# Kernel optimization log

Measured on AMD Instinct MI355X. Metric: run time of the kernel, lower is better.

Reference implementation:

```python
import jax, jax.numpy as jnp
import numpy as np

D_MODEL = 1024
H = 16
D_K = D_MODEL // H
B, S = 2, 2048
NEG = -1e9


def setup_inputs() -> dict:
    key = jax.random.key(0)
    ks = jax.random.split(key, 8)
    scale = 1.0 / np.sqrt(D_MODEL)
    q = jax.random.normal(ks[0], (B, S, D_MODEL), dtype=jnp.float32)
    k = jax.random.normal(ks[1], (B, S, D_MODEL), dtype=jnp.float32)
    v = jax.random.normal(ks[2], (B, S, D_MODEL), dtype=jnp.float32)
    # causal 0/1 mask, broadcastable to [B, h, S, S]
    mask = jnp.tril(jnp.ones((S, S), dtype=jnp.int32))[None, None, :, :]
    w_q = jax.random.normal(ks[3], (D_MODEL, D_MODEL), dtype=jnp.float32) * scale
    w_k = jax.random.normal(ks[4], (D_MODEL, D_MODEL), dtype=jnp.float32) * scale
    w_v = jax.random.normal(ks[5], (D_MODEL, D_MODEL), dtype=jnp.float32) * scale
    w_o = jax.random.normal(ks[6], (D_MODEL, D_MODEL), dtype=jnp.float32) * scale
    return {"q": q, "k": k, "v": v, "mask": mask,
            "w_q": w_q, "w_k": w_k, "w_v": w_v, "w_o": w_o}


def reference(q, k, v, mask, w_q, w_k, w_v, w_o):
    # projections (no bias)
    def split_heads(x):
        Bn, Sn, _ = x.shape
        return x.reshape(Bn, Sn, H, D_K).transpose(0, 2, 1, 3)  # [B,h,S,d_k]

    qh = split_heads(q @ w_q)
    kh = split_heads(k @ w_k)
    vh = split_heads(v @ w_v)

    scores = jnp.einsum('bhqd,bhkd->bhqk', qh, kh) / jnp.sqrt(
        jnp.asarray(D_K, dtype=qh.dtype))
    scores = jnp.where(mask == 0, jnp.asarray(NEG, dtype=scores.dtype), scores)
    attn = jax.nn.softmax(scores, axis=-1)  # dropout rate 0.0 -> identity
    x = jnp.einsum('bhqk,bhkd->bhqd', attn, vh)  # [B,h,S,d_k]
    x = x.transpose(0, 2, 1, 3).reshape(q.shape[0], q.shape[1], D_MODEL)
    return x @ w_o
```

## Files before the change

kernel.cpp:

```cpp
#include <hip/hip_runtime.h>

#define D_MODEL 1024
#define NH 16
#define DK 64
#define BB 2
#define SS 2048
#define M_TOT (BB*SS)

typedef float f32x4 __attribute__((ext_vector_type(4)));
typedef float f32x16 __attribute__((ext_vector_type(16)));
typedef __bf16 bf16x8 __attribute__((ext_vector_type(8)));
typedef unsigned int u32;

#define QSCALE 0.1803368801f
#define DEFER_THR 11.5416f

__device__ __forceinline__ unsigned short f2bf(float f){
  unsigned int u = __float_as_uint(f);
  unsigned int r = (u + 0x7fffu + ((u >> 16) & 1u)) >> 16;
  return (unsigned short)r;
}

__device__ __forceinline__ void gload_lds16(const void* g, void* l){
  __builtin_amdgcn_global_load_lds((const __attribute__((address_space(1))) void*)g,
                                   (__attribute__((address_space(3))) void*)l,
                                   16, 0, 0);
}

__device__ __forceinline__ void swap_half(u32 a, u32 b, int hi, u32& x, u32& y){
#if __has_builtin(__builtin_amdgcn_permlane32_swap)
  typedef unsigned int uint2v __attribute__((ext_vector_type(2)));
  uint2v r = __builtin_amdgcn_permlane32_swap(a, b, false, false);
  x = r.x; y = r.y;
#else
  u32 as = __shfl_xor(a, 32);
  u32 bs = __shfl_xor(b, 32);
  x = hi ? bs : a;
  y = hi ? b  : as;
#endif
}

__global__ __launch_bounds__(256) void cvt3_bf16(const float* __restrict__ q,
                                                 const float* __restrict__ k,
                                                 const float* __restrict__ v,
                                                 unsigned short* __restrict__ qb,
                                                 unsigned short* __restrict__ kb,
                                                 unsigned short* __restrict__ vb){
  const int which = blockIdx.y;
  const float* in = (which == 0) ? q : (which == 1) ? k : v;
  unsigned short* out = (which == 0) ? qb : (which == 1) ? kb : vb;
  int i = blockIdx.x * 256 + threadIdx.x;
  float4 f = ((const float4*)in)[i];
  ushort4 o;
  o.x = f2bf(f.x); o.y = f2bf(f.y); o.z = f2bf(f.z); o.w = f2bf(f.w);
  ((ushort4*)out)[i] = o;
}

__global__ __launch_bounds__(256) void transpose_cvt4(const float* __restrict__ wq,
                                                      const float* __restrict__ wk,
                                                      const float* __restrict__ wv,
                                                      const float* __restrict__ wo,
                                                      unsigned short* __restrict__ WqkvT,
                                                      unsigned short* __restrict__ woT){
  __shared__ float tile[64][65];
  const int which = blockIdx.z;
  const float* w = (which == 0) ? wq : (which == 1) ? wk : (which == 2) ? wv : wo;
  unsigned short* wt = (which == 3) ? woT : (WqkvT + (size_t)which * 1024 * 1024);
  const int N = D_MODEL;
  const int bx = blockIdx.x * 64;
  const int by = blockIdx.y * 64;
  const int t = threadIdx.x;
  #pragma unroll
  for (int i = 0; i < 16; ++i){
    int idx = t + i * 256;
    int r = idx >> 6, c = idx & 63;
    tile[r][c] = w[(size_t)(by + r) * N + bx + c];
  }
  __syncthreads();
  #pragma unroll
  for (int i = 0; i < 16; ++i){
    int idx = t + i * 256;
    int r = idx >> 6, c = idx & 63;
    wt[(size_t)(bx + r) * N + by + c] = f2bf(tile[c][r]);
  }
}

__global__ __launch_bounds__(256) void gemm_qkv(const unsigned short* __restrict__ Aq,
                                                const unsigned short* __restrict__ Ak,
                                                const unsigned short* __restrict__ Av,
                                                const unsigned short* __restrict__ WT,
                                                unsigned short* __restrict__ Qh,
                                                unsigned short* __restrict__ Kh,
                                                unsigned short* __restrict__ VhT){
  __shared__ unsigned short Al[2][128 * 32];
  __shared__ unsigned short Bl[2][128 * 32];
  const int tid = threadIdx.x;
  const int wid = tid >> 6, lane = tid & 63;
  const int lr = lane & 15, lg = lane >> 4;
  const int wm = wid >> 1, wn = wid & 1;
  const int bm = blockIdx.x, bn = blockIdx.y;
  const int seg = bn >> 3;
  const unsigned short* A = (seg == 0) ? Aq : (seg == 1) ? Ak : Av;
  const int K = D_MODEL;

  f32x4 acc[4][4];
  #pragma unroll
  for (int i = 0; i < 4; ++i)
    #pragma unroll
    for (int j = 0; j < 4; ++j)
      acc[i][j] = (f32x4){0.f, 0.f, 0.f, 0.f};

  auto stage = [&](int buf, int kt){
    #pragma unroll
    for (int r = 0; r < 2; ++r){
      int vt = tid + r * 256;
      int row = vt >> 2, c8 = (vt & 3) * 8;
      gload_lds16(A  + (size_t)(bm * 128 + row) * K + kt * 32 + c8,
                  &Al[buf][(wid << 9) + r * 2048]);
      gload_lds16(WT + (size_t)(bn * 128 + row) * K + kt * 32 + c8,
                  &Bl[buf][(wid << 9) + r * 2048]);
    }
  };

  stage(0, 0);
  int cur = 0;
  for (int kt = 0; kt < 32; ++kt){
    __syncthreads();
    if (kt + 1 < 32) stage(cur ^ 1, kt + 1);
    bf16x8 af[4], bfr[4];
    #pragma unroll
    for (int i = 0; i < 4; ++i)
      af[i] = *(const bf16x8*)&Al[cur][(wm * 64 + i * 16 + lr) * 32 + lg * 8];
    #pragma unroll
    for (int j = 0; j < 4; ++j)
      bfr[j] = *(const bf16x8*)&Bl[cur][(wn * 64 + j * 16 + lr) * 32 + lg * 8];
    #pragma unroll
    for (int i = 0; i < 4; ++i)
      #pragma unroll
      for (int j = 0; j < 4; ++j)
        acc[i][j] = __builtin_amdgcn_mfma_f32_16x16x32_bf16(af[i], bfr[j], acc[i][j], 0, 0, 0);
    cur ^= 1;
  }

  if (seg < 2){
    unsigned short* O = (seg == 0) ? Qh : Kh;
    const float sc = (seg == 0) ? QSCALE : 1.0f;
    #pragma unroll
    for (int i = 0; i < 4; ++i){
      int row0 = bm * 128 + wm * 64 + i * 16 + lg * 4;
      #pragma unroll
      for (int j = 0; j < 4; ++j){
        int colseg = (bn & 7) * 128 + wn * 64 + j * 16 + lr;
        int h = colseg >> 6, dk = colseg & 63;
        #pragma unroll
        for (int p = 0; p < 4; ++p){
          int rowm = row0 + p;
          int b = rowm >> 11, s = rowm & 2047;
          O[((size_t)(b * NH + h) * SS + s) * DK + dk] = f2bf(acc[i][j][p] * sc);
        }
      }
    }
  } else {
    #pragma unroll
    for (int i = 0; i < 4; ++i){
      int row0 = bm * 128 + wm * 64 + i * 16 + lg * 4;
      int b = row0 >> 11, s = row0 & 2047;
      #pragma unroll
      for (int j = 0; j < 4; ++j){
        int colseg = (bn & 7) * 128 + wn * 64 + j * 16 + lr;
        int h = colseg >> 6, dk = colseg & 63;
        ushort4 o4;
        o4.x = f2bf(acc[i][j][0]); o4.y = f2bf(acc[i][j][1]);
        o4.z = f2bf(acc[i][j][2]); o4.w = f2bf(acc[i][j][3]);
        *(ushort4*)&VhT[((size_t)(b * NH + h) * DK + dk) * SS + s] = o4;
      }
    }
  }
}

__global__ __launch_bounds__(256) void gemm_o64(const unsigned short* __restrict__ A,
                                                const unsigned short* __restrict__ Bt,
                                                float* __restrict__ O){
  __shared__ unsigned short Al[2][64 * 32];
  __shared__ unsigned short Bl[2][128 * 32];
  const int tid = threadIdx.x;
  const int wid = tid >> 6, lane = tid & 63;
  const int lr = lane & 15, lg = lane >> 4;
  const int wm = wid >> 1, wn = wid & 1;
  const int bm = blockIdx.x, bn = blockIdx.y;
  const int K = D_MODEL;

  f32x4 acc[2][4];
  #pragma unroll
  for (int i = 0; i < 2; ++i)
    #pragma unroll
    for (int j = 0; j < 4; ++j)
      acc[i][j] = (f32x4){0.f, 0.f, 0.f, 0.f};

  auto stage = [&](int buf, int kt){
    {
      int row = tid >> 2, c8 = (tid & 3) * 8;
      gload_lds16(A + (size_t)(bm * 64 + row) * K + kt * 32 + c8,
                  &Al[buf][wid << 9]);
    }
    #pragma unroll
    for (int r = 0; r < 2; ++r){
      int vt = tid + r * 256;
      int row = vt >> 2, c8 = (vt & 3) * 8;
      gload_lds16(Bt + (size_t)(bn * 128 + row) * K + kt * 32 + c8,
                  &Bl[buf][(wid << 9) + r * 2048]);
    }
  };

  stage(0, 0);
  int cur = 0;
  for (int kt = 0; kt < 32; ++kt){
    __syncthreads();
    if (kt + 1 < 32) stage(cur ^ 1, kt + 1);
    bf16x8 af[2], bfr[4];
    #pragma unroll
    for (int i = 0; i < 2; ++i)
      af[i] = *(const bf16x8*)&Al[cur][(wm * 32 + i * 16 + lr) * 32 + lg * 8];
    #pragma unroll
    for (int j = 0; j < 4; ++j)
      bfr[j] = *(const bf16x8*)&Bl[cur][(wn * 64 + j * 16 + lr) * 32 + lg * 8];
    #pragma unroll
    for (int i = 0; i < 2; ++i)
      #pragma unroll
      for (int j = 0; j < 4; ++j)
        acc[i][j] = __builtin_amdgcn_mfma_f32_16x16x32_bf16(af[i], bfr[j], acc[i][j], 0, 0, 0);
    cur ^= 1;
  }

  #pragma unroll
  for (int i = 0; i < 2; ++i){
    int row0 = bm * 64 + wm * 32 + i * 16 + lg * 4;
    #pragma unroll
    for (int j = 0; j < 4; ++j){
      int col = bn * 128 + wn * 64 + j * 16 + lr;
      #pragma unroll
      for (int p = 0; p < 4; ++p)
        O[(size_t)(row0 + p) * D_MODEL + col] = acc[i][j][p];
    }
  }
}

__global__ __launch_bounds__(256) void attn_kernel(const unsigned short* __restrict__ Qh,
                                                   const unsigned short* __restrict__ Kh,
                                                   const unsigned short* __restrict__ VhT,
                                                   unsigned short* __restrict__ Oc){
  __shared__ unsigned short SL[4][4096];
  const int bh = blockIdx.x;
  const int qblk = 31 - blockIdx.y;
  const int tid = threadIdx.x, wid = tid >> 6, lane = tid & 63;
  const int ln = lane & 31, hi = lane >> 5;
  const int qh = wid & 1, pp = wid >> 1;
  const int b = bh >> 4, h = bh & 15;
  const size_t kvbase = (size_t)bh * SS * DK;
  const int q0 = qblk * 64 + qh * 32;
  const int Tw = 2 * qblk + qh;
  const int R = (qblk + 2) >> 1;

  const unsigned short* qp = Qh + kvbase + (size_t)(q0 + ln) * DK + hi * 8;
  bf16x8 qbv[4];
  #pragma unroll
  for (int c = 0; c < 4; ++c) qbv[c] = *(const bf16x8*)(qp + c * 16);

  f32x16 oa0 = {0,0,0,0,0,0,0,0,0,0,0,0,0,0,0,0};
  f32x16 oa1 = {0,0,0,0,0,0,0,0,0,0,0,0,0,0,0,0};
  float m = -1e30f, ls = 0.f;

  #pragma unroll 1
  for (int r = 0; r < R; ++r){
    {
      const int k0A = (2 * r) * 64;
      const int k0B = k0A + 64;
      const bool haveB = (2 * r + 1) <= qblk;
      #pragma unroll
      for (int i = 0; i < 2; ++i){
        const int c = i * 256 + tid;
        const int row = c >> 3;
        const int slot = (c & 7) ^ (row & 7);
        const int ldso = (i * 256 + wid * 64) * 8;
        gload_lds16(Kh  + kvbase + (size_t)(k0A + row) * DK + slot * 8, &SL[0][ldso]);
        gload_lds16(VhT + kvbase + (size_t)row * SS + k0A + slot * 8,   &SL[1][ldso]);
        if (haveB){
          gload_lds16(Kh  + kvbase + (size_t)(k0B + row) * DK + slot * 8, &SL[2][ldso]);
          gload_lds16(VhT + kvbase + (size_t)row * SS + k0B + slot * 8,   &SL[3][ldso]);
        }
      }
    }
    __syncthreads();

    const int t = 2 * r + pp;
    if (t <= qblk){
      const unsigned short* Kb = SL[pp * 2];
      const unsigned short* Vb = SL[pp * 2 + 1];

      f32x16 sta = {0,0,0,0,0,0,0,0,0,0,0,0,0,0,0,0};
      f32x16 stb = {0,0,0,0,0,0,0,0,0,0,0,0,0,0,0,0};
      __builtin_amdgcn_s_setprio(1);
      #pragma unroll
      for (int c = 0; c < 4; ++c){
        const int po = ((c * 2 + hi) ^ (ln & 7)) * 8;
        bf16x8 kfa = *(const bf16x8*)&Kb[ln * 64 + po];
        bf16x8 kfb = *(const bf16x8*)&Kb[(32 + ln) * 64 + po];
        sta = __builtin_amdgcn_mfma_f32_32x32x16_bf16(kfa, qbv[c], sta, 0, 0, 0);
        stb = __builtin_amdgcn_mfma_f32_32x32x16_bf16(kfb, qbv[c], stb, 0, 0, 0);
      }
      __builtin_amdgcn_s_setprio(0);

      const int ta = 2 * t, tb = 2 * t + 1;
      if (tb == Tw){
        #pragma unroll
        for (int rr = 0; rr < 16; ++rr){
          int kg = (rr & 3) + 8 * (rr >> 2) + 4 * hi;
          if (kg > ln) stb[rr] = -1e30f;
        }
      } else if (ta == Tw){
        #pragma unroll
        for (int rr = 0; rr < 16; ++rr){
          int kg = (rr & 3) + 8 * (rr >> 2) + 4 * hi;
          if (kg > ln) sta[rr] = -1e30f;
          stb[rr] = -1e30f;
        }
      }

      float tm[8];
      #pragma unroll
      for (int i = 0; i < 8; ++i)
        tm[i] = fmaxf(fmaxf(sta[2*i], sta[2*i+1]), fmaxf(stb[2*i], stb[2*i+1]));
      float mx = fmaxf(fmaxf(fmaxf(tm[0], tm[1]), fmaxf(tm[2], tm[3])),
                       fmaxf(fmaxf(tm[4], tm[5]), fmaxf(tm[6], tm[7])));
      mx = fmaxf(mx, __shfl_xor(mx, 32));

      if (__any(mx > m + DEFER_THR)){
        const float mn = fmaxf(m, mx);
        const float fac = __builtin_amdgcn_exp2f(m - mn);
        m = mn;
        ls *= fac;
        #pragma unroll
        for (int rr = 0; rr < 16; ++rr){ oa0[rr] *= fac; oa1[rr] *= fac; }
      }

      #pragma unroll
      for (int rr = 0; rr < 16; ++rr){
        sta[rr] = __builtin_amdgcn_exp2f(sta[rr] - m);
        stb[rr] = __builtin_amdgcn_exp2f(stb[rr] - m);
      }
      float sm[8];
      #pragma unroll
      for (int i = 0; i < 8; ++i)
        sm[i] = (sta[2*i] + sta[2*i+1]) + (stb[2*i] + stb[2*i+1]);
      float rsum = ((sm[0] + sm[1]) + (sm[2] + sm[3])) + ((sm[4] + sm[5]) + (sm[6] + sm[7]));
      rsum += __shfl_xor(rsum, 32);
      ls += rsum;

      u32 ca[8], cb[8];
      #pragma unroll
      for (int i = 0; i < 8; ++i){
        asm("v_cvt_pk_bf16_f32 %0, %1, %2" : "=v"(ca[i]) : "v"(sta[2*i]), "v"(sta[2*i+1]));
        asm("v_cvt_pk_bf16_f32 %0, %1, %2" : "=v"(cb[i]) : "v"(stb[2*i]), "v"(stb[2*i+1]));
      }
      u32 w0[4], w1[4], w2[4], w3[4];
      swap_half(ca[0], ca[2], hi, w0[0], w0[2]);
      swap_half(ca[1], ca[3], hi, w0[1], w0[3]);
      swap_half(ca[4], ca[6], hi, w1[0], w1[2]);
      swap_half(ca[5], ca[7], hi, w1[1], w1[3]);
      swap_half(cb[0], cb[2], hi, w2[0], w2[2]);
      swap_half(cb[1], cb[3], hi, w2[1], w2[3]);
      swap_half(cb[4], cb[6], hi, w3[0], w3[2]);
      swap_half(cb[5], cb[7], hi, w3[1], w3[3]);
      bf16x8 pf[4];
      __builtin_memcpy(&pf[0], w0, 16);
      __builtin_memcpy(&pf[1], w1, 16);
      __builtin_memcpy(&pf[2], w2, 16);
      __builtin_memcpy(&pf[3], w3, 16);

      __builtin_amdgcn_s_setprio(1);
      #pragma unroll
      for (int ks = 0; ks < 4; ++ks){
        const int po = ((ks * 2 + hi) ^ (ln & 7)) * 8;
        bf16x8 v0 = *(const bf16x8*)&Vb[ln * 64 + po];
        bf16x8 v1 = *(const bf16x8*)&Vb[(32 + ln) * 64 + po];
        oa0 = __builtin_amdgcn_mfma_f32_32x32x16_bf16(v0, pf[ks], oa0, 0, 0, 0);
        oa1 = __builtin_amdgcn_mfma_f32_32x32x16_bf16(v1, pf[ks], oa1, 0, 0, 0);
      }
      __builtin_amdgcn_s_setprio(0);
    }
    __syncthreads();
  }

  float* oL  = (float*)&SL[0][0];
  float* mLs = (float*)&SL[2][0];
  if (wid >= 2){
    const int w = wid - 2;
    #pragma unroll
    for (int rr = 0; rr < 16; ++rr){
      oL[(w * 32 + rr) * 64 + lane]      = oa0[rr];
      oL[(w * 32 + 16 + rr) * 64 + lane] = oa1[rr];
    }
    if (hi == 0){ mLs[w * 32 + ln] = m; mLs[64 + w * 32 + ln] = ls; }
  }
  __syncthreads();
  if (wid < 2){
    const float m1  = mLs[wid * 32 + ln];
    const float ls1 = mLs[64 + wid * 32 + ln];
    const float mstar = fmaxf(m, m1);
    const float f0 = __builtin_amdgcn_exp2f(m  - mstar);
    const float f1 = __builtin_amdgcn_exp2f(m1 - mstar);
    const float inv = 1.0f / (f0 * ls + f1 * ls1);
    const size_t rowbase = ((size_t)b * SS + q0 + ln) * D_MODEL + h * DK;
    #pragma unroll
    for (int g = 0; g < 4; ++g){
      ushort4 o4;
      o4.x = f2bf((f0 * oa0[4*g + 0] + f1 * oL[(wid * 32 + 4*g + 0) * 64 + lane]) * inv);
      o4.y = f2bf((f0 * oa0[4*g + 1] + f1 * oL[(wid * 32 + 4*g + 1) * 64 + lane]) * inv);
      o4.z = f2bf((f0 * oa0[4*g + 2] + f1 * oL[(wid * 32 + 4*g + 2) * 64 + lane]) * inv);
      o4.w = f2bf((f0 * oa0[4*g + 3] + f1 * oL[(wid * 32 + 4*g + 3) * 64 + lane]) * inv);
      *(ushort4*)&Oc[rowbase + 8*g + 4*hi] = o4;
    }
    #pragma unroll
    for (int g = 0; g < 4; ++g){
      ushort4 o4;
      o4.x = f2bf((f0 * oa1[4*g + 0] + f1 * oL[(wid * 32 + 16 + 4*g + 0) * 64 + lane]) * inv);
      o4.y = f2bf((f0 * oa1[4*g + 1] + f1 * oL[(wid * 32 + 16 + 4*g + 1) * 64 + lane]) * inv);
      o4.z = f2bf((f0 * oa1[4*g + 2] + f1 * oL[(wid * 32 + 16 + 4*g + 2) * 64 + lane]) * inv);
      o4.w = f2bf((f0 * oa1[4*g + 3] + f1 * oL[(wid * 32 + 16 + 4*g + 3) * 64 + lane]) * inv);
      *(ushort4*)&Oc[rowbase + 32 + 8*g + 4*hi] = o4;
    }
  }
}

extern "C" void kernel_launch(void* const* d_in, const int* in_sizes, int n_in,
                              void* d_out, int out_size, void* d_ws, size_t ws_size,
                              hipStream_t stream){
  const float* q  = (const float*)d_in[0];
  const float* k  = (const float*)d_in[1];
  const float* v  = (const float*)d_in[2];
  const float* wq = (const float*)d_in[4];
  const float* wk = (const float*)d_in[5];
  const float* wv = (const float*)d_in[6];
  const float* wo = (const float*)d_in[7];
  float* out = (float*)d_out;

  char* ws = (char*)d_ws;
  const size_t MB = 1024 * 1024;
  unsigned short* qb     = (unsigned short*)(ws + 0 * MB);
  unsigned short* kb     = (unsigned short*)(ws + 8 * MB);
  unsigned short* vb     = (unsigned short*)(ws + 16 * MB);
  unsigned short* WqkvT  = (unsigned short*)(ws + 24 * MB);
  unsigned short* woT    = (unsigned short*)(ws + 30 * MB);
  unsigned short* Qh     = (unsigned short*)(ws + 32 * MB);
  unsigned short* Kh     = (unsigned short*)(ws + 40 * MB);
  unsigned short* VhT    = (unsigned short*)(ws + 48 * MB);
  unsigned short* attnb  = (unsigned short*)(ws + 56 * MB);

  const int n4 = (M_TOT * D_MODEL) / 4;
  dim3 gc(n4 / 256, 3);
  cvt3_bf16<<<gc, 256, 0, stream>>>(q, k, v, qb, kb, vb);

  dim3 tg(16, 16, 4);
  transpose_cvt4<<<tg, 256, 0, stream>>>(wq, wk, wv, wo, WqkvT, woT);

  dim3 gqkv(M_TOT / 128, 3 * D_MODEL / 128);
  gemm_qkv<<<gqkv, 256, 0, stream>>>(qb, kb, vb, WqkvT, Qh, Kh, VhT);

  dim3 ga(BB * NH, SS / 64);
  attn_kernel<<<ga, 256, 0, stream>>>(Qh, Kh, VhT, attnb);

  dim3 go(M_TOT / 64, D_MODEL / 128);
  gemm_o64<<<go, 256, 0, stream>>>(attnb, woT, out);
}
```

Measured before the change: 121.5 us.

## Prefetch K/V tiles into registers and remap query-block scheduling order

Replaces direct global-to-LDS async loads with register-staged prefetch. The next round's K/V tiles are loaded into registers while the current round computes, then written to swizzled LDS at the start of the next iteration. The query-block index mapping is also permuted so that heavy and light causal blocks interleave across the grid for better load balance. This costs extra registers per thread (32 dwords of staging), which may reduce occupancy, and the loads for the odd tile are now always issued even when that tile is unused.

```diff
diff --git a/kernel.cpp b/kernel.cpp
--- a/kernel.cpp
+++ b/kernel.cpp
@@ -251,7 +251,10 @@
                                                    unsigned short* __restrict__ Oc){
   __shared__ unsigned short SL[4][4096];
   const int bh = blockIdx.x;
-  const int qblk = 31 - blockIdx.y;
+  const int y = blockIdx.y;
+  const int am = y & 7, km = y >> 3;
+  const int qblk = (km == 0) ? am : (km == 1) ? (15 - am)
+                 : (km == 2) ? (16 + am) : (31 - am);
   const int tid = threadIdx.x, wid = tid >> 6, lane = tid & 63;
   const int ln = lane & 31, hi = lane >> 5;
   const int qh = wid & 1, pp = wid >> 1;
@@ -270,26 +273,36 @@
   f32x16 oa1 = {0,0,0,0,0,0,0,0,0,0,0,0,0,0,0,0};
   float m = -1e30f, ls = 0.f;
 
+  uint4 sKA[2], sVA[2], sKB[2], sVB[2];
+  const int c0  = tid,        c1  = 256 + tid;
+  const int rw0 = c0 >> 3,    rw1 = c1 >> 3;
+  const int s0  = c0 & 7,     s1  = c1 & 7;
+  const int w0o = rw0 * 64 + ((s0 ^ (rw0 & 7)) * 8);
+  const int w1o = rw1 * 64 + ((s1 ^ (rw1 & 7)) * 8);
+
+  auto load_st = [&](int r){
+    const int k0A = 2 * r * 64;
+    const int k0B = ((2 * r + 1) <= qblk) ? (k0A + 64) : k0A;
+    sKA[0] = *(const uint4*)&Kh [kvbase + (size_t)(k0A + rw0) * DK + s0 * 8];
+    sKA[1] = *(const uint4*)&Kh [kvbase + (size_t)(k0A + rw1) * DK + s1 * 8];
+    sVA[0] = *(const uint4*)&VhT[kvbase + (size_t)rw0 * SS + k0A + s0 * 8];
+    sVA[1] = *(const uint4*)&VhT[kvbase + (size_t)rw1 * SS + k0A + s1 * 8];
+    sKB[0] = *(const uint4*)&Kh [kvbase + (size_t)(k0B + rw0) * DK + s0 * 8];
+    sKB[1] = *(const uint4*)&Kh [kvbase + (size_t)(k0B + rw1) * DK + s1 * 8];
+    sVB[0] = *(const uint4*)&VhT[kvbase + (size_t)rw0 * SS + k0B + s0 * 8];
+    sVB[1] = *(const uint4*)&VhT[kvbase + (size_t)rw1 * SS + k0B + s1 * 8];
+  };
+
+  load_st(0);
+
   #pragma unroll 1
   for (int r = 0; r < R; ++r){
-    {
-      const int k0A = (2 * r) * 64;
-      const int k0B = k0A + 64;
-      const bool haveB = (2 * r + 1) <= qblk;
-      #pragma unroll
-      for (int i = 0; i < 2; ++i){
-        const int c = i * 256 + tid;
-        const int row = c >> 3;
-        const int slot = (c & 7) ^ (row & 7);
-        const int ldso = (i * 256 + wid * 64) * 8;
-        gload_lds16(Kh  + kvbase + (size_t)(k0A + row) * DK + slot * 8, &SL[0][ldso]);
-        gload_lds16(VhT + kvbase + (size_t)row * SS + k0A + slot * 8,   &SL[1][ldso]);
-        if (haveB){
-          gload_lds16(Kh  + kvbase + (size_t)(k0B + row) * DK + slot * 8, &SL[2][ldso]);
-          gload_lds16(VhT + kvbase + (size_t)row * SS + k0B + slot * 8,   &SL[3][ldso]);
-        }
-      }
-    }
+    __syncthreads();
+    *(uint4*)&SL[0][w0o] = sKA[0]; *(uint4*)&SL[0][w1o] = sKA[1];
+    *(uint4*)&SL[1][w0o] = sVA[0]; *(uint4*)&SL[1][w1o] = sVA[1];
+    *(uint4*)&SL[2][w0o] = sKB[0]; *(uint4*)&SL[2][w1o] = sKB[1];
+    *(uint4*)&SL[3][w0o] = sVB[0]; *(uint4*)&SL[3][w1o] = sVB[1];
+    if (r + 1 < R) load_st(r + 1);
     __syncthreads();
 
     const int t = 2 * r + pp;
@@ -388,8 +401,8 @@
       }
       __builtin_amdgcn_s_setprio(0);
     }
-    __syncthreads();
-  }
+  }
+  __syncthreads();
 
   float* oL  = (float*)&SL[0][0];
   float* mLs = (float*)&SL[2][0];
```

Result: slower. 180.5 us (+48.6%).
